# Kernel tuning notes

Hardware: AMD Instinct MI355X
Metric: run time of the kernel (lower is better)

Reference implementation:

```python
import jax, jax.numpy as jnp
import numpy as np

WIN = 8          # window side
N = WIN * WIN    # tokens per window = 64
C = 180          # channels
H = 6            # heads
D = C // H       # head dim = 30


def _relative_index():
    coords = jnp.stack(jnp.meshgrid(jnp.arange(WIN), jnp.arange(WIN), indexing='ij'))
    coords = coords.reshape(2, -1)                       # (2, N)
    rel = coords[:, :, None] - coords[:, None, :]        # (2, N, N)
    idx = (rel[0] + WIN - 1) * (2 * WIN - 1) + (rel[1] + WIN - 1)
    return idx.reshape(-1)                               # (N*N,) int


def setup_inputs() -> dict:
    key = jax.random.key(0)
    ks = jax.random.split(key, 6)
    B, WNum = 4096, 1024
    windows = jax.random.normal(ks[0], (B, N, C), dtype=jnp.float32)
    mask = jax.random.normal(ks[1], (WNum, N, N), dtype=jnp.float32)
    w_qkv = jax.random.normal(ks[2], (C, 3 * C), dtype=jnp.float32) * 0.02
    bias_table = jax.random.normal(ks[3], ((2 * WIN - 1) ** 2, H), dtype=jnp.float32) * 0.02
    w_proj = jax.random.normal(ks[4], (C, C), dtype=jnp.float32) * 0.02
    b_proj = jnp.zeros((C,), dtype=jnp.float32)
    return {"windows": windows, "mask": mask, "w_qkv": w_qkv,
            "bias_table": bias_table, "w_proj": w_proj, "b_proj": b_proj}


def reference(windows, mask, w_qkv, bias_table, w_proj, b_proj):
    B, n, c = windows.shape
    WNum = mask.shape[0]
    rel_idx = _relative_index()

    # qkv projection: (B, N, 3C) -> (3, B, H, N, D)
    qkv = (windows @ w_qkv).reshape(B, n, 3, H, D).transpose(2, 0, 3, 1, 4)
    q, k, v = qkv[0], qkv[1], qkv[2]

    scale = 1.0 / jnp.sqrt(jnp.float32(D))
    scores = jnp.einsum('bhnd,bhmd->bhnm', q, k) * scale     # (B, H, N, N)

    # relative position bias gather: (N*N, H) -> (H, N, N)
    rel_bias = bias_table[rel_idx].reshape(n, n, H).transpose(2, 0, 1)
    scores = scores + rel_bias[None]

    # per-window mask add
    scores = scores.reshape(B // WNum, WNum, H, n, n) + mask[None, :, None, :, :]
    scores = scores.reshape(B, H, n, n)

    attn = jax.nn.softmax(scores, axis=-1)
    out = jnp.einsum('bhnm,bhmd->bhnd', attn, v)             # (B, H, N, D)
    z = out.transpose(0, 2, 1, 3).reshape(B, n, c)
    return z @ w_proj + b_proj
```

## Files before the change

### kernel.cpp

```cpp
#include <hip/hip_runtime.h>


typedef __bf16 bf16;
typedef bf16 bf16x8 __attribute__((ext_vector_type(8)));
typedef float f32x4 __attribute__((ext_vector_type(4)));

#define MFMA(a, b, c) __builtin_amdgcn_mfma_f32_16x16x32_bf16(a, b, c, 0, 0, 0)

__global__ void prep_w(const float* __restrict__ wqkv,
                       const float* __restrict__ wproj,
                       const float* __restrict__ btab,
                       bf16* __restrict__ wqkvT,
                       bf16* __restrict__ wprojT,
                       float* __restrict__ relb)
{
    const int idx = blockIdx.x * 256 + threadIdx.x;
    if (idx < 110592) {
        const int oc = idx / 192, kk = idx - oc * 192;
        const int h = oc / 96, r = oc - h * 96;
        const int sec = r >> 5, d = r & 31;
        wqkvT[idx] = (bf16)((kk < 180 && d < 30) ? wqkv[kk * 540 + sec * 180 + h * 30 + d] : 0.f);
    } else if (idx < 147456) {
        const int r = idx - 110592;
        const int n = r / 192, k = r - n * 192;
        wprojT[r] = (bf16)((n < 180 && k < 180) ? wproj[k * 180 + n] : 0.f);
    } else if (idx < 172032) {
        const int r = idx - 147456;
        const int h = r >> 12;
        const int ij = r & 4095;
        const int i = ij >> 6, j = ij & 63;
        const int rel = ((i >> 3) - (j >> 3) + 7) * 15 + ((i & 7) - (j & 7) + 7);
        relb[r] = btab[rel * 6 + h];
    }
}

__global__ __launch_bounds__(384, 4)
void swin_mfma(const float* __restrict__ xg_all,
               const float* __restrict__ mask_all,
               const float* __restrict__ bproj,
               const bf16* __restrict__ wqkvT,
               const bf16* __restrict__ wprojT,
               const float* __restrict__ relb,
               float* __restrict__ outg)
{
    __shared__ __align__(16) short xb[64 * 200];

    const int b    = blockIdx.x;
    const int tid  = threadIdx.x;
    const int w    = tid >> 6;
    const int lane = tid & 63;
    const int l15  = lane & 15;
    const int g    = lane >> 4;

    const float* xg    = xg_all + (size_t)b * 11520;
    const float* maskw = mask_all + (size_t)(b & 1023) * 4096;

    {
        float4 xv[7];
        #pragma unroll
        for (int u = 0; u < 7; u++)
            xv[u] = *reinterpret_cast<const float4*>(xg + 4 * (tid + 384 * u));
        float4 xt;
        if (tid < 192) xt = *reinterpret_cast<const float4*>(xg + 4 * (2688 + tid));
        for (int e = tid; e < 640; e += 384) {
            const int i = e / 10;
            ((unsigned*)(xb + i * 200 + 180))[e - i * 10] = 0u;
        }
        #pragma unroll
        for (int u = 0; u < 7; u++) {
            const int e = tid + 384 * u;
            const int i = e / 45;
            const int c = 4 * e - i * 180;
            const unsigned p0 = (unsigned)__builtin_bit_cast(unsigned short, (bf16)xv[u].x)
                              | ((unsigned)__builtin_bit_cast(unsigned short, (bf16)xv[u].y) << 16);
            const unsigned p1 = (unsigned)__builtin_bit_cast(unsigned short, (bf16)xv[u].z)
                              | ((unsigned)__builtin_bit_cast(unsigned short, (bf16)xv[u].w) << 16);
            *reinterpret_cast<unsigned*>(xb + i * 200 + c)     = p0;
            *reinterpret_cast<unsigned*>(xb + i * 200 + c + 2) = p1;
        }
        if (tid < 192) {
            const int e = 2688 + tid;
            const int i = e / 45;
            const int c = 4 * e - i * 180;
            const unsigned p0 = (unsigned)__builtin_bit_cast(unsigned short, (bf16)xt.x)
                              | ((unsigned)__builtin_bit_cast(unsigned short, (bf16)xt.y) << 16);
            const unsigned p1 = (unsigned)__builtin_bit_cast(unsigned short, (bf16)xt.z)
                              | ((unsigned)__builtin_bit_cast(unsigned short, (bf16)xt.w) << 16);
            *reinterpret_cast<unsigned*>(xb + i * 200 + c)     = p0;
            *reinterpret_cast<unsigned*>(xb + i * 200 + c + 2) = p1;
        }
    }
    __syncthreads();

    const bf16* wqh = wqkvT + (size_t)(w * 96) * 192;
    const int rowoff = l15 * 192 + 8 * g;

    bf16x8 qf[4], kf[4];
    {
        f32x4 aqk[4][4];
        #pragma unroll
        for (int ct = 0; ct < 4; ct++)
            #pragma unroll
            for (int tt = 0; tt < 4; tt++) aqk[ct][tt] = (f32x4)0.f;
        #pragma unroll
        for (int ks = 0; ks < 6; ks++) {
            bf16x8 xf[4];
            #pragma unroll
            for (int tt = 0; tt < 4; tt++)
                xf[tt] = *reinterpret_cast<const bf16x8*>(xb + (16 * tt + l15) * 200 + 32 * ks + 8 * g);
            __builtin_amdgcn_s_setprio(1);
            #pragma unroll
            for (int ct = 0; ct < 4; ct++) {
                const bf16x8 wf = *reinterpret_cast<const bf16x8*>(wqh + ct * 3072 + rowoff + 32 * ks);
                #pragma unroll
                for (int tt = 0; tt < 4; tt++)
                    aqk[ct][tt] = MFMA(wf, xf[tt], aqk[ct][tt]);
            }
            __builtin_amdgcn_s_setprio(0);
        }
        #pragma unroll
        for (int tt = 0; tt < 4; tt++)
            #pragma unroll
            for (int s = 0; s < 8; s++) {
                qf[tt][s] = (bf16)(aqk[s >> 2][tt][s & 3] * 0.18257418583505537f);
                kf[tt][s] = (bf16)(aqk[2 + (s >> 2)][tt][s & 3]);
            }
    }
    __builtin_amdgcn_sched_barrier(0);

    bf16x8 pf[4][2];
    {
        const float* relh = relb + w * 4096;
        f32x4 bc[4];
        {
            const float* rbb = relh + l15 * 64 + 4 * g;
            const float* mkb = maskw + l15 * 64 + 4 * g;
            #pragma unroll
            for (int jt = 0; jt < 4; jt++) {
                const float4 rb = *reinterpret_cast<const float4*>(rbb + 16 * jt);
                const float4 mk = *reinterpret_cast<const float4*>(mkb + 16 * jt);
                bc[jt][0] = rb.x + mk.x; bc[jt][1] = rb.y + mk.y;
                bc[jt][2] = rb.z + mk.z; bc[jt][3] = rb.w + mk.w;
            }
        }
        #pragma unroll
        for (int it = 0; it < 4; it++) {
            f32x4 stj[4];
            __builtin_amdgcn_s_setprio(1);
            #pragma unroll
            for (int jt = 0; jt < 4; jt++) stj[jt] = MFMA(kf[jt], qf[it], bc[jt]);
            __builtin_amdgcn_s_setprio(0);

            f32x4 bn[4];
            if (it < 3) {
                const int i1 = 16 * (it + 1) + l15;
                const float* rbb = relh + i1 * 64 + 4 * g;
                const float* mkb = maskw + i1 * 64 + 4 * g;
                #pragma unroll
                for (int jt = 0; jt < 4; jt++) {
                    const float4 rb = *reinterpret_cast<const float4*>(rbb + 16 * jt);
                    const float4 mk = *reinterpret_cast<const float4*>(mkb + 16 * jt);
                    bn[jt][0] = rb.x + mk.x; bn[jt][1] = rb.y + mk.y;
                    bn[jt][2] = rb.z + mk.z; bn[jt][3] = rb.w + mk.w;
                }
            }

            float sum = 0.f;
            #pragma unroll
            for (int jt = 0; jt < 4; jt++) {
                const float e0 = __expf(stj[jt][0]);
                const float e1 = __expf(stj[jt][1]);
                const float e2 = __expf(stj[jt][2]);
                const float e3 = __expf(stj[jt][3]);
                stj[jt][0] = e0; stj[jt][1] = e1; stj[jt][2] = e2; stj[jt][3] = e3;
                sum += (e0 + e1) + (e2 + e3);
            }
            sum += __shfl_xor(sum, 16);
            sum += __shfl_xor(sum, 32);
            const float inv = 1.0f / sum;
            #pragma unroll
            for (int k2 = 0; k2 < 2; k2++)
                #pragma unroll
                for (int s = 0; s < 8; s++)
                    pf[it][k2][s] = (bf16)(stj[2 * k2 + (s >> 2)][s & 3] * inv);

            if (it < 3) {
                #pragma unroll
                for (int jt = 0; jt < 4; jt++) bc[jt] = bn[jt];
            }
        }
    }
    __builtin_amdgcn_sched_barrier(0);

    bf16x8 vf[2][2];
    {
        f32x4 av[4][2];
        #pragma unroll
        for (int tt = 0; tt < 4; tt++) { av[tt][0] = (f32x4)0.f; av[tt][1] = (f32x4)0.f; }
        #pragma unroll
        for (int ks = 0; ks < 6; ks++) {
            bf16x8 xf[4];
            #pragma unroll
            for (int tt = 0; tt < 4; tt++)
                xf[tt] = *reinterpret_cast<const bf16x8*>(xb + (16 * tt + l15) * 200 + 32 * ks + 8 * g);
            __builtin_amdgcn_s_setprio(1);
            #pragma unroll
            for (int cv = 0; cv < 2; cv++) {
                const bf16x8 wf = *reinterpret_cast<const bf16x8*>(wqh + (4 + cv) * 3072 + rowoff + 32 * ks);
                #pragma unroll
                for (int tt = 0; tt < 4; tt++)
                    av[tt][cv] = MFMA(xf[tt], wf, av[tt][cv]);
            }
            __builtin_amdgcn_s_setprio(0);
        }
        #pragma unroll
        for (int cv = 0; cv < 2; cv++)
            #pragma unroll
            for (int k2 = 0; k2 < 2; k2++)
                #pragma unroll
                for (int s = 0; s < 8; s++)
                    vf[cv][k2][s] = (bf16)(av[2 * k2 + (s >> 2)][cv][s & 3]);
    }
    __builtin_amdgcn_sched_barrier(0);

    f32x4 zacc[4][2];
    #pragma unroll
    for (int it = 0; it < 4; it++) { zacc[it][0] = (f32x4)0.f; zacc[it][1] = (f32x4)0.f; }
    __builtin_amdgcn_s_setprio(1);
    #pragma unroll
    for (int k2 = 0; k2 < 2; k2++)
        #pragma unroll
        for (int cv = 0; cv < 2; cv++)
            #pragma unroll
            for (int it = 0; it < 4; it++)
                zacc[it][cv] = MFMA(pf[it][k2], vf[cv][k2], zacc[it][cv]);
    __builtin_amdgcn_s_setprio(0);

    __syncthreads();
    #pragma unroll
    for (int cv = 0; cv < 2; cv++) {
        const int d = 16 * cv + l15;
        if (d < 30) {
            #pragma unroll
            for (int it = 0; it < 4; it++)
                #pragma unroll
                for (int r = 0; r < 4; r++)
                    xb[(16 * it + 4 * g + r) * 200 + w * 30 + d] =
                        __builtin_bit_cast(short, (bf16)zacc[it][cv][r]);
        }
    }
    __syncthreads();

    f32x4 pa[4][2];
    #pragma unroll
    for (int mt = 0; mt < 4; mt++) { pa[mt][0] = (f32x4)0.f; pa[mt][1] = (f32x4)0.f; }
    #pragma unroll
    for (int ks = 0; ks < 6; ks++) {
        bf16x8 zf[4];
        #pragma unroll
        for (int mt = 0; mt < 4; mt++)
            zf[mt] = *reinterpret_cast<const bf16x8*>(xb + (16 * mt + l15) * 200 + 32 * ks + 8 * g);
        __builtin_amdgcn_s_setprio(1);
        #pragma unroll
        for (int q2 = 0; q2 < 2; q2++) {
            const bf16x8 wf = *reinterpret_cast<const bf16x8*>(
                wprojT + ((2 * w + q2) * 16 + l15) * 192 + 32 * ks + 8 * g);
            #pragma unroll
            for (int mt = 0; mt < 4; mt++)
                pa[mt][q2] = MFMA(zf[mt], wf, pa[mt][q2]);
        }
        __builtin_amdgcn_s_setprio(0);
    }
    #pragma unroll
    for (int q2 = 0; q2 < 2; q2++) {
        const int n = (2 * w + q2) * 16 + l15;
        if (n < 180) {
            const float bn = bproj[n];
            float* const ob = outg + (size_t)b * 11520 + n;
            #pragma unroll
            for (int mt = 0; mt < 4; mt++)
                #pragma unroll
                for (int r = 0; r < 4; r++)
                    ob[(16 * mt + 4 * g + r) * 180] = pa[mt][q2][r] + bn;
        }
    }
}

extern "C" void kernel_launch(void* const* d_in, const int* in_sizes, int n_in,
                              void* d_out, int out_size, void* d_ws, size_t ws_size,
                              hipStream_t stream) {
    const float* windows = (const float*)d_in[0];
    const float* mask    = (const float*)d_in[1];
    const float* wqkv    = (const float*)d_in[2];
    const float* btab    = (const float*)d_in[3];
    const float* wproj   = (const float*)d_in[4];
    const float* bproj   = (const float*)d_in[5];

    bf16*  wqkvT  = (bf16*)d_ws;
    bf16*  wprojT = (bf16*)((char*)d_ws + 221184);
    float* relb   = (float*)((char*)d_ws + 294912);

    hipLaunchKernelGGL(prep_w, dim3(672), dim3(256), 0, stream,
                       wqkv, wproj, btab, wqkvT, wprojT, relb);
    hipLaunchKernelGGL(swin_mfma, dim3(4096), dim3(384), 0, stream,
                       windows, mask, bproj, wqkvT, wprojT, relb, (float*)d_out);
}
```

Before: 285.9 us.

## Process four same-mask windows per block with double-buffered LDS prefetch

```diff
diff --git a/kernel.cpp b/kernel.cpp
--- a/kernel.cpp
+++ b/kernel.cpp
@@ -34,6 +34,11 @@
     }
 }
 
+__device__ __forceinline__ unsigned pack2(float a, float b) {
+    return (unsigned)__builtin_bit_cast(unsigned short, (bf16)a)
+         | ((unsigned)__builtin_bit_cast(unsigned short, (bf16)b) << 16);
+}
+
 __global__ __launch_bounds__(384, 4)
 void swin_mfma(const float* __restrict__ xg_all,
                const float* __restrict__ mask_all,
@@ -43,7 +48,7 @@
                const float* __restrict__ relb,
                float* __restrict__ outg)
 {
-    __shared__ __align__(16) short xb[64 * 200];
+    __shared__ __align__(16) short xb2[2][64 * 200];
 
     const int b    = blockIdx.x;
     const int tid  = threadIdx.x;
@@ -52,237 +57,267 @@
     const int l15  = lane & 15;
     const int g    = lane >> 4;
 
-    const float* xg    = xg_all + (size_t)b * 11520;
-    const float* maskw = mask_all + (size_t)(b & 1023) * 4096;
-
+    const float* maskw = mask_all + (size_t)b * 4096;
+    const bf16*  wqh   = wqkvT + (size_t)(w * 96) * 192;
+    const int rowoff   = l15 * 192 + 8 * g;
+    const float* relh  = relb + w * 4096;
+
+    for (int e = tid; e < 1280; e += 384) {
+        const int bi = (e >= 640) ? 1 : 0;
+        const int e2 = e - bi * 640;
+        const int i = e2 / 10;
+        ((unsigned*)(&xb2[bi][0] + i * 200 + 180))[e2 - i * 10] = 0u;
+    }
     {
+        const float* xg = xg_all + (size_t)b * 11520;
         float4 xv[7];
         #pragma unroll
         for (int u = 0; u < 7; u++)
             xv[u] = *reinterpret_cast<const float4*>(xg + 4 * (tid + 384 * u));
         float4 xt;
         if (tid < 192) xt = *reinterpret_cast<const float4*>(xg + 4 * (2688 + tid));
-        for (int e = tid; e < 640; e += 384) {
-            const int i = e / 10;
-            ((unsigned*)(xb + i * 200 + 180))[e - i * 10] = 0u;
-        }
         #pragma unroll
         for (int u = 0; u < 7; u++) {
             const int e = tid + 384 * u;
             const int i = e / 45;
             const int c = 4 * e - i * 180;
-            const unsigned p0 = (unsigned)__builtin_bit_cast(unsigned short, (bf16)xv[u].x)
-                              | ((unsigned)__builtin_bit_cast(unsigned short, (bf16)xv[u].y) << 16);
-            const unsigned p1 = (unsigned)__builtin_bit_cast(unsigned short, (bf16)xv[u].z)
-                              | ((unsigned)__builtin_bit_cast(unsigned short, (bf16)xv[u].w) << 16);
-            *reinterpret_cast<unsigned*>(xb + i * 200 + c)     = p0;
-            *reinterpret_cast<unsigned*>(xb + i * 200 + c + 2) = p1;
+            *reinterpret_cast<unsigned*>(&xb2[0][0] + i * 200 + c)     = pack2(xv[u].x, xv[u].y);
+            *reinterpret_cast<unsigned*>(&xb2[0][0] + i * 200 + c + 2) = pack2(xv[u].z, xv[u].w);
         }
         if (tid < 192) {
             const int e = 2688 + tid;
             const int i = e / 45;
             const int c = 4 * e - i * 180;
-            const unsigned p0 = (unsigned)__builtin_bit_cast(unsigned short, (bf16)xt.x)
-                              | ((unsigned)__builtin_bit_cast(unsigned short, (bf16)xt.y) << 16);
-            const unsigned p1 = (unsigned)__builtin_bit_cast(unsigned short, (bf16)xt.z)
-                              | ((unsigned)__builtin_bit_cast(unsigned short, (bf16)xt.w) << 16);
-            *reinterpret_cast<unsigned*>(xb + i * 200 + c)     = p0;
-            *reinterpret_cast<unsigned*>(xb + i * 200 + c + 2) = p1;
+            *reinterpret_cast<unsigned*>(&xb2[0][0] + i * 200 + c)     = pack2(xt.x, xt.y);
+            *reinterpret_cast<unsigned*>(&xb2[0][0] + i * 200 + c + 2) = pack2(xt.z, xt.w);
         }
     }
     __syncthreads();
 
-    const bf16* wqh = wqkvT + (size_t)(w * 96) * 192;
-    const int rowoff = l15 * 192 + 8 * g;
-
-    bf16x8 qf[4], kf[4];
-    {
-        f32x4 aqk[4][4];
-        #pragma unroll
-        for (int ct = 0; ct < 4; ct++)
-            #pragma unroll
-            for (int tt = 0; tt < 4; tt++) aqk[ct][tt] = (f32x4)0.f;
-        #pragma unroll
-        for (int ks = 0; ks < 6; ks++) {
-            bf16x8 xf[4];
+    int cur = 0;
+    #pragma unroll 1
+    for (int wi = 0; wi < 4; ++wi) {
+        short* const xb = &xb2[cur][0];
+        const int bw = b + 1024 * wi;
+
+        bf16x8 qf[4], kf[4];
+        {
+            f32x4 aqk[4][4];
+            #pragma unroll
+            for (int ct = 0; ct < 4; ct++)
+                #pragma unroll
+                for (int tt = 0; tt < 4; tt++) aqk[ct][tt] = (f32x4)0.f;
+            #pragma unroll
+            for (int ks = 0; ks < 6; ks++) {
+                bf16x8 xf[4];
+                #pragma unroll
+                for (int tt = 0; tt < 4; tt++)
+                    xf[tt] = *reinterpret_cast<const bf16x8*>(xb + (16 * tt + l15) * 200 + 32 * ks + 8 * g);
+                __builtin_amdgcn_s_setprio(1);
+                #pragma unroll
+                for (int ct = 0; ct < 4; ct++) {
+                    const bf16x8 wf = *reinterpret_cast<const bf16x8*>(wqh + ct * 3072 + rowoff + 32 * ks);
+                    #pragma unroll
+                    for (int tt = 0; tt < 4; tt++)
+                        aqk[ct][tt] = MFMA(wf, xf[tt], aqk[ct][tt]);
+                }
+                __builtin_amdgcn_s_setprio(0);
+            }
             #pragma unroll
             for (int tt = 0; tt < 4; tt++)
-                xf[tt] = *reinterpret_cast<const bf16x8*>(xb + (16 * tt + l15) * 200 + 32 * ks + 8 * g);
-            __builtin_amdgcn_s_setprio(1);
-            #pragma unroll
-            for (int ct = 0; ct < 4; ct++) {
-                const bf16x8 wf = *reinterpret_cast<const bf16x8*>(wqh + ct * 3072 + rowoff + 32 * ks);
-                #pragma unroll
-                for (int tt = 0; tt < 4; tt++)
-                    aqk[ct][tt] = MFMA(wf, xf[tt], aqk[ct][tt]);
-            }
-            __builtin_amdgcn_s_setprio(0);
-        }
-        #pragma unroll
-        for (int tt = 0; tt < 4; tt++)
-            #pragma unroll
-            for (int s = 0; s < 8; s++) {
-                qf[tt][s] = (bf16)(aqk[s >> 2][tt][s & 3] * 0.18257418583505537f);
-                kf[tt][s] = (bf16)(aqk[2 + (s >> 2)][tt][s & 3]);
-            }
-    }
-    __builtin_amdgcn_sched_barrier(0);
-
-    bf16x8 pf[4][2];
-    {
-        const float* relh = relb + w * 4096;
-        f32x4 bc[4];
+                #pragma unroll
+                for (int s = 0; s < 8; s++) {
+                    qf[tt][s] = (bf16)(aqk[s >> 2][tt][s & 3] * 0.18257418583505537f);
+                    kf[tt][s] = (bf16)(aqk[2 + (s >> 2)][tt][s & 3]);
+                }
+        }
+        __builtin_amdgcn_sched_barrier(0);
+
+        bf16x8 pf[4][2];
         {
-            const float* rbb = relh + l15 * 64 + 4 * g;
-            const float* mkb = maskw + l15 * 64 + 4 * g;
-            #pragma unroll
-            for (int jt = 0; jt < 4; jt++) {
-                const float4 rb = *reinterpret_cast<const float4*>(rbb + 16 * jt);
-                const float4 mk = *reinterpret_cast<const float4*>(mkb + 16 * jt);
-                bc[jt][0] = rb.x + mk.x; bc[jt][1] = rb.y + mk.y;
-                bc[jt][2] = rb.z + mk.z; bc[jt][3] = rb.w + mk.w;
-            }
-        }
-        #pragma unroll
-        for (int it = 0; it < 4; it++) {
-            f32x4 stj[4];
-            __builtin_amdgcn_s_setprio(1);
-            #pragma unroll
-            for (int jt = 0; jt < 4; jt++) stj[jt] = MFMA(kf[jt], qf[it], bc[jt]);
-            __builtin_amdgcn_s_setprio(0);
-
-            f32x4 bn[4];
-            if (it < 3) {
-                const int i1 = 16 * (it + 1) + l15;
-                const float* rbb = relh + i1 * 64 + 4 * g;
-                const float* mkb = maskw + i1 * 64 + 4 * g;
+            f32x4 bc[4];
+            {
+                const float* rbb = relh + l15 * 64 + 4 * g;
+                const float* mkb = maskw + l15 * 64 + 4 * g;
                 #pragma unroll
                 for (int jt = 0; jt < 4; jt++) {
                     const float4 rb = *reinterpret_cast<const float4*>(rbb + 16 * jt);
                     const float4 mk = *reinterpret_cast<const float4*>(mkb + 16 * jt);
-                    bn[jt][0] = rb.x + mk.x; bn[jt][1] = rb.y + mk.y;
-                    bn[jt][2] = rb.z + mk.z; bn[jt][3] = rb.w + mk.w;
-                }
-            }
-
-            float sum = 0.f;
-            #pragma unroll
-            for (int jt = 0; jt < 4; jt++) {
-                const float e0 = __expf(stj[jt][0]);
-                const float e1 = __expf(stj[jt][1]);
-                const float e2 = __expf(stj[jt][2]);
-                const float e3 = __expf(stj[jt][3]);
-                stj[jt][0] = e0; stj[jt][1] = e1; stj[jt][2] = e2; stj[jt][3] = e3;
-                sum += (e0 + e1) + (e2 + e3);
-            }
-            sum += __shfl_xor(sum, 16);
-            sum += __shfl_xor(sum, 32);
-            const float inv = 1.0f / sum;
-            #pragma unroll
-            for (int k2 = 0; k2 < 2; k2++)
-                #pragma unroll
-                for (int s = 0; s < 8; s++)
-                    pf[it][k2][s] = (bf16)(stj[2 * k2 + (s >> 2)][s & 3] * inv);
-
-            if (it < 3) {
-                #pragma unroll
-                for (int jt = 0; jt < 4; jt++) bc[jt] = bn[jt];
-            }
-        }
-    }
-    __builtin_amdgcn_sched_barrier(0);
-
-    bf16x8 vf[2][2];
-    {
-        f32x4 av[4][2];
-        #pragma unroll
-        for (int tt = 0; tt < 4; tt++) { av[tt][0] = (f32x4)0.f; av[tt][1] = (f32x4)0.f; }
+                    bc[jt][0] = rb.x + mk.x; bc[jt][1] = rb.y + mk.y;
+                    bc[jt][2] = rb.z + mk.z; bc[jt][3] = rb.w + mk.w;
+                }
+            }
+            #pragma unroll
+            for (int it = 0; it < 4; it++) {
+                f32x4 stj[4];
+                __builtin_amdgcn_s_setprio(1);
+                #pragma unroll
+                for (int jt = 0; jt < 4; jt++) stj[jt] = MFMA(kf[jt], qf[it], bc[jt]);
+                __builtin_amdgcn_s_setprio(0);
+
+                f32x4 bn[4];
+                if (it < 3) {
+                    const int i1 = 16 * (it + 1) + l15;
+                    const float* rbb = relh + i1 * 64 + 4 * g;
+                    const float* mkb = maskw + i1 * 64 + 4 * g;
+                    #pragma unroll
+                    for (int jt = 0; jt < 4; jt++) {
+                        const float4 rb = *reinterpret_cast<const float4*>(rbb + 16 * jt);
+                        const float4 mk = *reinterpret_cast<const float4*>(mkb + 16 * jt);
+                        bn[jt][0] = rb.x + mk.x; bn[jt][1] = rb.y + mk.y;
+                        bn[jt][2] = rb.z + mk.z; bn[jt][3] = rb.w + mk.w;
+                    }
+                }
+
+                float sum = 0.f;
+                #pragma unroll
+                for (int jt = 0; jt < 4; jt++) {
+                    const float e0 = __expf(stj[jt][0]);
+                    const float e1 = __expf(stj[jt][1]);
+                    const float e2 = __expf(stj[jt][2]);
+                    const float e3 = __expf(stj[jt][3]);
+                    stj[jt][0] = e0; stj[jt][1] = e1; stj[jt][2] = e2; stj[jt][3] = e3;
+                    sum += (e0 + e1) + (e2 + e3);
+                }
+                sum += __shfl_xor(sum, 16);
+                sum += __shfl_xor(sum, 32);
+                const float inv = 1.0f / sum;
+                #pragma unroll
+                for (int k2 = 0; k2 < 2; k2++)
+                    #pragma unroll
+                    for (int s = 0; s < 8; s++)
+                        pf[it][k2][s] = (bf16)(stj[2 * k2 + (s >> 2)][s & 3] * inv);
+
+                if (it < 3) {
+                    #pragma unroll
+                    for (int jt = 0; jt < 4; jt++) bc[jt] = bn[jt];
+                }
+            }
+        }
+        __builtin_amdgcn_sched_barrier(0);
+
+        bf16x8 vf[2][2];
+        {
+            f32x4 av[4][2];
+            #pragma unroll
+            for (int tt = 0; tt < 4; tt++) { av[tt][0] = (f32x4)0.f; av[tt][1] = (f32x4)0.f; }
+            #pragma unroll
+            for (int ks = 0; ks < 6; ks++) {
+                bf16x8 xf[4];
+                #pragma unroll
+                for (int tt = 0; tt < 4; tt++)
+                    xf[tt] = *reinterpret_cast<const bf16x8*>(xb + (16 * tt + l15) * 200 + 32 * ks + 8 * g);
+                __builtin_amdgcn_s_setprio(1);
+                #pragma unroll
+                for (int cv = 0; cv < 2; cv++) {
+                    const bf16x8 wf = *reinterpret_cast<const bf16x8*>(wqh + (4 + cv) * 3072 + rowoff + 32 * ks);
+                    #pragma unroll
+                    for (int tt = 0; tt < 4; tt++)
+                        av[tt][cv] = MFMA(xf[tt], wf, av[tt][cv]);
+                }
+                __builtin_amdgcn_s_setprio(0);
+            }
+            #pragma unroll
+            for (int cv = 0; cv < 2; cv++)
+                #pragma unroll
+                for (int k2 = 0; k2 < 2; k2++)
+                    #pragma unroll
+                    for (int s = 0; s < 8; s++)
+                        vf[cv][k2][s] = (bf16)(av[2 * k2 + (s >> 2)][cv][s & 3]);
+        }
+        __builtin_amdgcn_sched_barrier(0);
+
+        f32x4 zacc[4][2];
+        #pragma unroll
+        for (int it = 0; it < 4; it++) { zacc[it][0] = (f32x4)0.f; zacc[it][1] = (f32x4)0.f; }
+        __builtin_amdgcn_s_setprio(1);
+        #pragma unroll
+        for (int k2 = 0; k2 < 2; k2++)
+            #pragma unroll
+            for (int cv = 0; cv < 2; cv++)
+                #pragma unroll
+                for (int it = 0; it < 4; it++)
+                    zacc[it][cv] = MFMA(pf[it][k2], vf[cv][k2], zacc[it][cv]);
+        __builtin_amdgcn_s_setprio(0);
+
+        __syncthreads();
+        #pragma unroll
+        for (int cv = 0; cv < 2; cv++) {
+            const int d = 16 * cv + l15;
+            if (d < 30) {
+                #pragma unroll
+                for (int it = 0; it < 4; it++)
+                    #pragma unroll
+                    for (int r = 0; r < 4; r++)
+                        xb[(16 * it + 4 * g + r) * 200 + w * 30 + d] =
+                            __builtin_bit_cast(short, (bf16)zacc[it][cv][r]);
+            }
+        }
+        __syncthreads();
+
+        float4 nxv[7], nxt;
+        if (wi < 3) {
+            const float* xgn = xg_all + (size_t)(bw + 1024) * 11520;
+            #pragma unroll
+            for (int u = 0; u < 7; u++)
+                nxv[u] = *reinterpret_cast<const float4*>(xgn + 4 * (tid + 384 * u));
+            if (tid < 192) nxt = *reinterpret_cast<const float4*>(xgn + 4 * (2688 + tid));
+        }
+
+        f32x4 pa[4][2];
+        #pragma unroll
+        for (int mt = 0; mt < 4; mt++) { pa[mt][0] = (f32x4)0.f; pa[mt][1] = (f32x4)0.f; }
         #pragma unroll
         for (int ks = 0; ks < 6; ks++) {
-            bf16x8 xf[4];
-            #pragma unroll
-            for (int tt = 0; tt < 4; tt++)
-                xf[tt] = *reinterpret_cast<const bf16x8*>(xb + (16 * tt + l15) * 200 + 32 * ks + 8 * g);
+            bf16x8 zf[4];
+            #pragma unroll
+            for (int mt = 0; mt < 4; mt++)
+                zf[mt] = *reinterpret_cast<const bf16x8*>(xb + (16 * mt + l15) * 200 + 32 * ks + 8 * g);
             __builtin_amdgcn_s_setprio(1);
             #pragma unroll
-            for (int cv = 0; cv < 2; cv++) {
-                const bf16x8 wf = *reinterpret_cast<const bf16x8*>(wqh + (4 + cv) * 3072 + rowoff + 32 * ks);
-                #pragma unroll
-                for (int tt = 0; tt < 4; tt++)
-                    av[tt][cv] = MFMA(xf[tt], wf, av[tt][cv]);
+            for (int q2 = 0; q2 < 2; q2++) {
+                const bf16x8 wf = *reinterpret_cast<const bf16x8*>(
+                    wprojT + ((2 * w + q2) * 16 + l15) * 192 + 32 * ks + 8 * g);
+                #pragma unroll
+                for (int mt = 0; mt < 4; mt++)
+                    pa[mt][q2] = MFMA(zf[mt], wf, pa[mt][q2]);
             }
             __builtin_amdgcn_s_setprio(0);
         }
         #pragma unroll
-        for (int cv = 0; cv < 2; cv++)
-            #pragma unroll
-            for (int k2 = 0; k2 < 2; k2++)
-                #pragma unroll
-                for (int s = 0; s < 8; s++)
-                    vf[cv][k2][s] = (bf16)(av[2 * k2 + (s >> 2)][cv][s & 3]);
-    }
-    __builtin_amdgcn_sched_barrier(0);
-
-    f32x4 zacc[4][2];
-    #pragma unroll
-    for (int it = 0; it < 4; it++) { zacc[it][0] = (f32x4)0.f; zacc[it][1] = (f32x4)0.f; }
-    __builtin_amdgcn_s_setprio(1);
-    #pragma unroll
-    for (int k2 = 0; k2 < 2; k2++)
-        #pragma unroll
-        for (int cv = 0; cv < 2; cv++)
-            #pragma unroll
-            for (int it = 0; it < 4; it++)
-                zacc[it][cv] = MFMA(pf[it][k2], vf[cv][k2], zacc[it][cv]);
-    __builtin_amdgcn_s_setprio(0);
-
-    __syncthreads();
-    #pragma unroll
-    for (int cv = 0; cv < 2; cv++) {
-        const int d = 16 * cv + l15;
-        if (d < 30) {
-            #pragma unroll
-            for (int it = 0; it < 4; it++)
-                #pragma unroll
-                for (int r = 0; r < 4; r++)
-                    xb[(16 * it + 4 * g + r) * 200 + w * 30 + d] =
-                        __builtin_bit_cast(short, (bf16)zacc[it][cv][r]);
-        }
-    }
-    __syncthreads();
-
-    f32x4 pa[4][2];
-    #pragma unroll
-    for (int mt = 0; mt < 4; mt++) { pa[mt][0] = (f32x4)0.f; pa[mt][1] = (f32x4)0.f; }
-    #pragma unroll
-    for (int ks = 0; ks < 6; ks++) {
-        bf16x8 zf[4];
-        #pragma unroll
-        for (int mt = 0; mt < 4; mt++)
-            zf[mt] = *reinterpret_cast<const bf16x8*>(xb + (16 * mt + l15) * 200 + 32 * ks + 8 * g);
-        __builtin_amdgcn_s_setprio(1);
-        #pragma unroll
         for (int q2 = 0; q2 < 2; q2++) {
-            const bf16x8 wf = *reinterpret_cast<const bf16x8*>(
-                wprojT + ((2 * w + q2) * 16 + l15) * 192 + 32 * ks + 8 * g);
-            #pragma unroll
-            for (int mt = 0; mt < 4; mt++)
-                pa[mt][q2] = MFMA(zf[mt], wf, pa[mt][q2]);
-        }
-        __builtin_amdgcn_s_setprio(0);
-    }
-    #pragma unroll
-    for (int q2 = 0; q2 < 2; q2++) {
-        const int n = (2 * w + q2) * 16 + l15;
-        if (n < 180) {
-            const float bn = bproj[n];
-            float* const ob = outg + (size_t)b * 11520 + n;
-            #pragma unroll
-            for (int mt = 0; mt < 4; mt++)
-                #pragma unroll
-                for (int r = 0; r < 4; r++)
-                    ob[(16 * mt + 4 * g + r) * 180] = pa[mt][q2][r] + bn;
-        }
+            const int n = (2 * w + q2) * 16 + l15;
+            if (n < 180) {
+                const float bn = bproj[n];
+                float* const ob = outg + (size_t)bw * 11520 + n;
+                #pragma unroll
+                for (int mt = 0; mt < 4; mt++)
+                    #pragma unroll
+                    for (int r = 0; r < 4; r++)
+                        ob[(16 * mt + 4 * g + r) * 180] = pa[mt][q2][r] + bn;
+            }
+        }
+
+        if (wi < 3) {
+            short* const nb = &xb2[cur ^ 1][0];
+            #pragma unroll
+            for (int u = 0; u < 7; u++) {
+                const int e = tid + 384 * u;
+                const int i = e / 45;
+                const int c = 4 * e - i * 180;
+                *reinterpret_cast<unsigned*>(nb + i * 200 + c)     = pack2(nxv[u].x, nxv[u].y);
+                *reinterpret_cast<unsigned*>(nb + i * 200 + c + 2) = pack2(nxv[u].z, nxv[u].w);
+            }
+            if (tid < 192) {
+                const int e = 2688 + tid;
+                const int i = e / 45;
+                const int c = 4 * e - i * 180;
+                *reinterpret_cast<unsigned*>(nb + i * 200 + c)     = pack2(nxt.x, nxt.y);
+                *reinterpret_cast<unsigned*>(nb + i * 200 + c + 2) = pack2(nxt.z, nxt.w);
+            }
+        }
+        __syncthreads();
+        cur ^= 1;
     }
 }
 
@@ -302,6 +337,6 @@
 
     hipLaunchKernelGGL(prep_w, dim3(672), dim3(256), 0, stream,
                        wqkv, wproj, btab, wqkvT, wprojT, relb);
-    hipLaunchKernelGGL(swin_mfma, dim3(4096), dim3(384), 0, stream,
+    hipLaunchKernelGGL(swin_mfma, dim3(1024), dim3(384), 0, stream,
                        windows, mask, bproj, wqkvT, wprojT, relb, (float*)d_out);
 }
```

Measured after the change: 645.6 us. 126% more time.

## Add 3-wave kernel processing two heads per wave with global z scratch

Applied to the files above, without the earlier changes.

```diff
diff --git a/kernel.cpp b/kernel.cpp
--- a/kernel.cpp
+++ b/kernel.cpp
@@ -34,14 +34,264 @@
     }
 }
 
+__device__ __forceinline__ unsigned pack2(float a, float b) {
+    return (unsigned)__builtin_bit_cast(unsigned short, (bf16)a)
+         | ((unsigned)__builtin_bit_cast(unsigned short, (bf16)b) << 16);
+}
+
+__global__ __launch_bounds__(192, 4)
+void swin_mfma3(const float* __restrict__ xg_all,
+                const float* __restrict__ mask_all,
+                const float* __restrict__ bproj,
+                const bf16* __restrict__ wqkvT,
+                const bf16* __restrict__ wprojT,
+                const float* __restrict__ relb,
+                bf16* __restrict__ zws,
+                float* __restrict__ outg)
+{
+    __shared__ __align__(16) short xb[64 * 200];
+
+    const int b    = blockIdx.x;
+    const int tid  = threadIdx.x;
+    const int wq   = tid >> 6;
+    const int lane = tid & 63;
+    const int l15  = lane & 15;
+    const int g    = lane >> 4;
+
+    const float* xg    = xg_all + (size_t)b * 11520;
+    const float* maskw = mask_all + (size_t)(b & 1023) * 4096;
+    bf16* const  zw    = zws + (size_t)b * 12288;
+
+    {
+        float4 xv[15];
+        #pragma unroll
+        for (int u = 0; u < 15; u++)
+            xv[u] = *reinterpret_cast<const float4*>(xg + 4 * (tid + 192 * u));
+        for (int e = tid; e < 640; e += 192) {
+            const int i = e / 10;
+            ((unsigned*)(xb + i * 200 + 180))[e - i * 10] = 0u;
+        }
+        #pragma unroll
+        for (int u = 0; u < 15; u++) {
+            const int e = tid + 192 * u;
+            const int i = e / 45;
+            const int c = 4 * e - i * 180;
+            *reinterpret_cast<unsigned*>(xb + i * 200 + c)     = pack2(xv[u].x, xv[u].y);
+            *reinterpret_cast<unsigned*>(xb + i * 200 + c + 2) = pack2(xv[u].z, xv[u].w);
+        }
+    }
+    __syncthreads();
+
+    #pragma unroll 1
+    for (int hh = 0; hh < 2; ++hh) {
+        const int h = 2 * wq + hh;
+        const bf16* wqh = wqkvT + (size_t)(h * 96) * 192;
+        const float* relh = relb + h * 4096;
+        const int rowoff = l15 * 192 + 8 * g;
+
+        bf16x8 qf[4], kf[4];
+        {
+            f32x4 aqk[4][4];
+            #pragma unroll
+            for (int ct = 0; ct < 4; ct++)
+                #pragma unroll
+                for (int tt = 0; tt < 4; tt++) aqk[ct][tt] = (f32x4)0.f;
+            #pragma unroll
+            for (int ks = 0; ks < 6; ks++) {
+                bf16x8 xf[4];
+                #pragma unroll
+                for (int tt = 0; tt < 4; tt++)
+                    xf[tt] = *reinterpret_cast<const bf16x8*>(xb + (16 * tt + l15) * 200 + 32 * ks + 8 * g);
+                __builtin_amdgcn_s_setprio(1);
+                #pragma unroll
+                for (int ct = 0; ct < 4; ct++) {
+                    const bf16x8 wf = *reinterpret_cast<const bf16x8*>(wqh + ct * 3072 + rowoff + 32 * ks);
+                    #pragma unroll
+                    for (int tt = 0; tt < 4; tt++)
+                        aqk[ct][tt] = MFMA(wf, xf[tt], aqk[ct][tt]);
+                }
+                __builtin_amdgcn_s_setprio(0);
+            }
+            #pragma unroll
+            for (int tt = 0; tt < 4; tt++)
+                #pragma unroll
+                for (int s = 0; s < 8; s++) {
+                    qf[tt][s] = (bf16)(aqk[s >> 2][tt][s & 3] * 0.18257418583505537f);
+                    kf[tt][s] = (bf16)(aqk[2 + (s >> 2)][tt][s & 3]);
+                }
+        }
+        __builtin_amdgcn_sched_barrier(0);
+
+        bf16x8 pf[4][2];
+        {
+            f32x4 bc[4];
+            {
+                const float* rbb = relh + l15 * 64 + 4 * g;
+                const float* mkb = maskw + l15 * 64 + 4 * g;
+                #pragma unroll
+                for (int jt = 0; jt < 4; jt++) {
+                    const float4 rb = *reinterpret_cast<const float4*>(rbb + 16 * jt);
+                    const float4 mk = *reinterpret_cast<const float4*>(mkb + 16 * jt);
+                    bc[jt][0] = rb.x + mk.x; bc[jt][1] = rb.y + mk.y;
+                    bc[jt][2] = rb.z + mk.z; bc[jt][3] = rb.w + mk.w;
+                }
+            }
+            #pragma unroll
+            for (int it = 0; it < 4; it++) {
+                f32x4 stj[4];
+                __builtin_amdgcn_s_setprio(1);
+                #pragma unroll
+                for (int jt = 0; jt < 4; jt++) stj[jt] = MFMA(kf[jt], qf[it], bc[jt]);
+                __builtin_amdgcn_s_setprio(0);
+
+                f32x4 bn[4];
+                if (it < 3) {
+                    const int i1 = 16 * (it + 1) + l15;
+                    const float* rbb = relh + i1 * 64 + 4 * g;
+                    const float* mkb = maskw + i1 * 64 + 4 * g;
+                    #pragma unroll
+                    for (int jt = 0; jt < 4; jt++) {
+                        const float4 rb = *reinterpret_cast<const float4*>(rbb + 16 * jt);
+                        const float4 mk = *reinterpret_cast<const float4*>(mkb + 16 * jt);
+                        bn[jt][0] = rb.x + mk.x; bn[jt][1] = rb.y + mk.y;
+                        bn[jt][2] = rb.z + mk.z; bn[jt][3] = rb.w + mk.w;
+                    }
+                }
+
+                float sum = 0.f;
+                #pragma unroll
+                for (int jt = 0; jt < 4; jt++) {
+                    const float e0 = __expf(stj[jt][0]);
+                    const float e1 = __expf(stj[jt][1]);
+                    const float e2 = __expf(stj[jt][2]);
+                    const float e3 = __expf(stj[jt][3]);
+                    stj[jt][0] = e0; stj[jt][1] = e1; stj[jt][2] = e2; stj[jt][3] = e3;
+                    sum += (e0 + e1) + (e2 + e3);
+                }
+                sum += __shfl_xor(sum, 16);
+                sum += __shfl_xor(sum, 32);
+                const float inv = 1.0f / sum;
+                #pragma unroll
+                for (int k2 = 0; k2 < 2; k2++)
+                    #pragma unroll
+                    for (int s = 0; s < 8; s++)
+                        pf[it][k2][s] = (bf16)(stj[2 * k2 + (s >> 2)][s & 3] * inv);
+
+                if (it < 3) {
+                    #pragma unroll
+                    for (int jt = 0; jt < 4; jt++) bc[jt] = bn[jt];
+                }
+            }
+        }
+        __builtin_amdgcn_sched_barrier(0);
+
+        bf16x8 vf[2][2];
+        {
+            f32x4 av[4][2];
+            #pragma unroll
+            for (int tt = 0; tt < 4; tt++) { av[tt][0] = (f32x4)0.f; av[tt][1] = (f32x4)0.f; }
+            #pragma unroll
+            for (int ks = 0; ks < 6; ks++) {
+                bf16x8 xf[4];
+                #pragma unroll
+                for (int tt = 0; tt < 4; tt++)
+                    xf[tt] = *reinterpret_cast<const bf16x8*>(xb + (16 * tt + l15) * 200 + 32 * ks + 8 * g);
+                __builtin_amdgcn_s_setprio(1);
+                #pragma unroll
+                for (int cv = 0; cv < 2; cv++) {
+                    const bf16x8 wf = *reinterpret_cast<const bf16x8*>(wqh + (4 + cv) * 3072 + rowoff + 32 * ks);
+                    #pragma unroll
+                    for (int tt = 0; tt < 4; tt++)
+                        av[tt][cv] = MFMA(xf[tt], wf, av[tt][cv]);
+                }
+                __builtin_amdgcn_s_setprio(0);
+            }
+            #pragma unroll
+            for (int cv = 0; cv < 2; cv++)
+                #pragma unroll
+                for (int k2 = 0; k2 < 2; k2++)
+                    #pragma unroll
+                    for (int s = 0; s < 8; s++)
+                        vf[cv][k2][s] = (bf16)(av[2 * k2 + (s >> 2)][cv][s & 3]);
+        }
+        __builtin_amdgcn_sched_barrier(0);
+
+        f32x4 zacc[4][2];
+        #pragma unroll
+        for (int it = 0; it < 4; it++) { zacc[it][0] = (f32x4)0.f; zacc[it][1] = (f32x4)0.f; }
+        __builtin_amdgcn_s_setprio(1);
+        #pragma unroll
+        for (int k2 = 0; k2 < 2; k2++)
+            #pragma unroll
+            for (int cv = 0; cv < 2; cv++)
+                #pragma unroll
+                for (int it = 0; it < 4; it++)
+                    zacc[it][cv] = MFMA(pf[it][k2], vf[cv][k2], zacc[it][cv]);
+        __builtin_amdgcn_s_setprio(0);
+
+        #pragma unroll
+        for (int cv = 0; cv < 2; cv++) {
+            const int d = 16 * cv + l15;
+            if (d < 30) {
+                #pragma unroll
+                for (int it = 0; it < 4; it++)
+                    #pragma unroll
+                    for (int r = 0; r < 4; r++)
+                        zw[(16 * it + 4 * g + r) * 192 + h * 30 + d] = (bf16)zacc[it][cv][r];
+            }
+        }
+        __builtin_amdgcn_sched_barrier(0);
+    }
+    __syncthreads();
+
+    {
+        f32x4 pa[4][4];
+        #pragma unroll
+        for (int mt = 0; mt < 4; mt++)
+            #pragma unroll
+            for (int q3 = 0; q3 < 4; q3++) pa[mt][q3] = (f32x4)0.f;
+        #pragma unroll
+        for (int ks = 0; ks < 6; ks++) {
+            bf16x8 zf[4];
+            #pragma unroll
+            for (int mt = 0; mt < 4; mt++)
+                zf[mt] = *reinterpret_cast<const bf16x8*>(zw + (16 * mt + l15) * 192 + 32 * ks + 8 * g);
+            __builtin_amdgcn_s_setprio(1);
+            #pragma unroll
+            for (int q3 = 0; q3 < 4; q3++) {
+                const int nt = 4 * wq + q3;
+                const bf16x8 wf = *reinterpret_cast<const bf16x8*>(
+                    wprojT + (nt * 16 + l15) * 192 + 32 * ks + 8 * g);
+                #pragma unroll
+                for (int mt = 0; mt < 4; mt++)
+                    pa[mt][q3] = MFMA(zf[mt], wf, pa[mt][q3]);
+            }
+            __builtin_amdgcn_s_setprio(0);
+        }
+        #pragma unroll
+        for (int q3 = 0; q3 < 4; q3++) {
+            const int n = (4 * wq + q3) * 16 + l15;
+            if (n < 180) {
+                const float bn = bproj[n];
+                float* const ob = outg + (size_t)b * 11520 + n;
+                #pragma unroll
+                for (int mt = 0; mt < 4; mt++)
+                    #pragma unroll
+                    for (int r = 0; r < 4; r++)
+                        ob[(16 * mt + 4 * g + r) * 180] = pa[mt][q3][r] + bn;
+            }
+        }
+    }
+}
+
 __global__ __launch_bounds__(384, 4)
-void swin_mfma(const float* __restrict__ xg_all,
-               const float* __restrict__ mask_all,
-               const float* __restrict__ bproj,
-               const bf16* __restrict__ wqkvT,
-               const bf16* __restrict__ wprojT,
-               const float* __restrict__ relb,
-               float* __restrict__ outg)
+void swin_mfma6(const float* __restrict__ xg_all,
+                const float* __restrict__ mask_all,
+                const float* __restrict__ bproj,
+                const bf16* __restrict__ wqkvT,
+                const bf16* __restrict__ wprojT,
+                const float* __restrict__ relb,
+                float* __restrict__ outg)
 {
     __shared__ __align__(16) short xb[64 * 200];
 
@@ -71,23 +321,15 @@
             const int e = tid + 384 * u;
             const int i = e / 45;
             const int c = 4 * e - i * 180;
-            const unsigned p0 = (unsigned)__builtin_bit_cast(unsigned short, (bf16)xv[u].x)
-                              | ((unsigned)__builtin_bit_cast(unsigned short, (bf16)xv[u].y) << 16);
-            const unsigned p1 = (unsigned)__builtin_bit_cast(unsigned short, (bf16)xv[u].z)
-                              | ((unsigned)__builtin_bit_cast(unsigned short, (bf16)xv[u].w) << 16);
-            *reinterpret_cast<unsigned*>(xb + i * 200 + c)     = p0;
-            *reinterpret_cast<unsigned*>(xb + i * 200 + c + 2) = p1;
+            *reinterpret_cast<unsigned*>(xb + i * 200 + c)     = pack2(xv[u].x, xv[u].y);
+            *reinterpret_cast<unsigned*>(xb + i * 200 + c + 2) = pack2(xv[u].z, xv[u].w);
         }
         if (tid < 192) {
             const int e = 2688 + tid;
             const int i = e / 45;
             const int c = 4 * e - i * 180;
-            const unsigned p0 = (unsigned)__builtin_bit_cast(unsigned short, (bf16)xt.x)
-                              | ((unsigned)__builtin_bit_cast(unsigned short, (bf16)xt.y) << 16);
-            const unsigned p1 = (unsigned)__builtin_bit_cast(unsigned short, (bf16)xt.z)
-                              | ((unsigned)__builtin_bit_cast(unsigned short, (bf16)xt.w) << 16);
-            *reinterpret_cast<unsigned*>(xb + i * 200 + c)     = p0;
-            *reinterpret_cast<unsigned*>(xb + i * 200 + c + 2) = p1;
+            *reinterpret_cast<unsigned*>(xb + i * 200 + c)     = pack2(xt.x, xt.y);
+            *reinterpret_cast<unsigned*>(xb + i * 200 + c + 2) = pack2(xt.z, xt.w);
         }
     }
     __syncthreads();
@@ -299,9 +541,17 @@
     bf16*  wqkvT  = (bf16*)d_ws;
     bf16*  wprojT = (bf16*)((char*)d_ws + 221184);
     float* relb   = (float*)((char*)d_ws + 294912);
+    bf16*  zws    = (bf16*)((char*)d_ws + 393216);
+
+    const bool ws_ok = ws_size >= (size_t)393216 + (size_t)4096 * 12288 * 2;
 
     hipLaunchKernelGGL(prep_w, dim3(672), dim3(256), 0, stream,
                        wqkv, wproj, btab, wqkvT, wprojT, relb);
-    hipLaunchKernelGGL(swin_mfma, dim3(4096), dim3(384), 0, stream,
-                       windows, mask, bproj, wqkvT, wprojT, relb, (float*)d_out);
+    if (ws_ok) {
+        hipLaunchKernelGGL(swin_mfma3, dim3(4096), dim3(192), 0, stream,
+                           windows, mask, bproj, wqkvT, wprojT, relb, zws, (float*)d_out);
+    } else {
+        hipLaunchKernelGGL(swin_mfma6, dim3(4096), dim3(384), 0, stream,
+                           windows, mask, bproj, wqkvT, wprojT, relb, (float*)d_out);
+    }
 }
```

New measurement: 471.4 us. +64.9%, slower.

## Compute V before softmax and fuse PV MFMA per row tile

Applied to the files above, without the earlier changes.

```diff
diff --git a/kernel.cpp b/kernel.cpp
--- a/kernel.cpp
+++ b/kernel.cpp
@@ -34,6 +34,11 @@
     }
 }
 
+__device__ __forceinline__ unsigned pack2(float a, float b) {
+    return (unsigned)__builtin_bit_cast(unsigned short, (bf16)a)
+         | ((unsigned)__builtin_bit_cast(unsigned short, (bf16)b) << 16);
+}
+
 __global__ __launch_bounds__(384, 4)
 void swin_mfma(const float* __restrict__ xg_all,
                const float* __restrict__ mask_all,
@@ -71,23 +76,15 @@
             const int e = tid + 384 * u;
             const int i = e / 45;
             const int c = 4 * e - i * 180;
-            const unsigned p0 = (unsigned)__builtin_bit_cast(unsigned short, (bf16)xv[u].x)
-                              | ((unsigned)__builtin_bit_cast(unsigned short, (bf16)xv[u].y) << 16);
-            const unsigned p1 = (unsigned)__builtin_bit_cast(unsigned short, (bf16)xv[u].z)
-                              | ((unsigned)__builtin_bit_cast(unsigned short, (bf16)xv[u].w) << 16);
-            *reinterpret_cast<unsigned*>(xb + i * 200 + c)     = p0;
-            *reinterpret_cast<unsigned*>(xb + i * 200 + c + 2) = p1;
+            *reinterpret_cast<unsigned*>(xb + i * 200 + c)     = pack2(xv[u].x, xv[u].y);
+            *reinterpret_cast<unsigned*>(xb + i * 200 + c + 2) = pack2(xv[u].z, xv[u].w);
         }
         if (tid < 192) {
             const int e = 2688 + tid;
             const int i = e / 45;
             const int c = 4 * e - i * 180;
-            const unsigned p0 = (unsigned)__builtin_bit_cast(unsigned short, (bf16)xt.x)
-                              | ((unsigned)__builtin_bit_cast(unsigned short, (bf16)xt.y) << 16);
-            const unsigned p1 = (unsigned)__builtin_bit_cast(unsigned short, (bf16)xt.z)
-                              | ((unsigned)__builtin_bit_cast(unsigned short, (bf16)xt.w) << 16);
-            *reinterpret_cast<unsigned*>(xb + i * 200 + c)     = p0;
-            *reinterpret_cast<unsigned*>(xb + i * 200 + c + 2) = p1;
+            *reinterpret_cast<unsigned*>(xb + i * 200 + c)     = pack2(xt.x, xt.y);
+            *reinterpret_cast<unsigned*>(xb + i * 200 + c + 2) = pack2(xt.z, xt.w);
         }
     }
     __syncthreads();
@@ -128,113 +125,90 @@
     }
     __builtin_amdgcn_sched_barrier(0);
 
-    bf16x8 pf[4][2];
+    bf16x8 vf[2][2];
+    {
+        f32x4 av[4][2];
+        #pragma unroll
+        for (int tt = 0; tt < 4; tt++) { av[tt][0] = (f32x4)0.f; av[tt][1] = (f32x4)0.f; }
+        #pragma unroll
+        for (int ks = 0; ks < 6; ks++) {
+            bf16x8 xf[4];
+            #pragma unroll
+            for (int tt = 0; tt < 4; tt++)
+                xf[tt] = *reinterpret_cast<const bf16x8*>(xb + (16 * tt + l15) * 200 + 32 * ks + 8 * g);
+            __builtin_amdgcn_s_setprio(1);
+            #pragma unroll
+            for (int cv = 0; cv < 2; cv++) {
+                const bf16x8 wf = *reinterpret_cast<const bf16x8*>(wqh + (4 + cv) * 3072 + rowoff + 32 * ks);
+                #pragma unroll
+                for (int tt = 0; tt < 4; tt++)
+                    av[tt][cv] = MFMA(xf[tt], wf, av[tt][cv]);
+            }
+            __builtin_amdgcn_s_setprio(0);
+        }
+        #pragma unroll
+        for (int cv = 0; cv < 2; cv++)
+            #pragma unroll
+            for (int k2 = 0; k2 < 2; k2++)
+                #pragma unroll
+                for (int s = 0; s < 8; s++)
+                    vf[cv][k2][s] = (bf16)(av[2 * k2 + (s >> 2)][cv][s & 3]);
+    }
+    __builtin_amdgcn_sched_barrier(0);
+
+    f32x4 zacc[4][2];
+    #pragma unroll
+    for (int it = 0; it < 4; it++) { zacc[it][0] = (f32x4)0.f; zacc[it][1] = (f32x4)0.f; }
     {
         const float* relh = relb + w * 4096;
-        f32x4 bc[4];
-        {
-            const float* rbb = relh + l15 * 64 + 4 * g;
-            const float* mkb = maskw + l15 * 64 + 4 * g;
+        #pragma unroll
+        for (int it = 0; it < 4; it++) {
+            const int i = 16 * it + l15;
+            const float* rbb = relh + i * 64 + 4 * g;
+            const float* mkb = maskw + i * 64 + 4 * g;
+            float4 rb[4], mk[4];
             #pragma unroll
             for (int jt = 0; jt < 4; jt++) {
-                const float4 rb = *reinterpret_cast<const float4*>(rbb + 16 * jt);
-                const float4 mk = *reinterpret_cast<const float4*>(mkb + 16 * jt);
-                bc[jt][0] = rb.x + mk.x; bc[jt][1] = rb.y + mk.y;
-                bc[jt][2] = rb.z + mk.z; bc[jt][3] = rb.w + mk.w;
-            }
-        }
-        #pragma unroll
-        for (int it = 0; it < 4; it++) {
+                rb[jt] = *reinterpret_cast<const float4*>(rbb + 16 * jt);
+                mk[jt] = *reinterpret_cast<const float4*>(mkb + 16 * jt);
+            }
+
             f32x4 stj[4];
             __builtin_amdgcn_s_setprio(1);
             #pragma unroll
-            for (int jt = 0; jt < 4; jt++) stj[jt] = MFMA(kf[jt], qf[it], bc[jt]);
-            __builtin_amdgcn_s_setprio(0);
-
-            f32x4 bn[4];
-            if (it < 3) {
-                const int i1 = 16 * (it + 1) + l15;
-                const float* rbb = relh + i1 * 64 + 4 * g;
-                const float* mkb = maskw + i1 * 64 + 4 * g;
-                #pragma unroll
-                for (int jt = 0; jt < 4; jt++) {
-                    const float4 rb = *reinterpret_cast<const float4*>(rbb + 16 * jt);
-                    const float4 mk = *reinterpret_cast<const float4*>(mkb + 16 * jt);
-                    bn[jt][0] = rb.x + mk.x; bn[jt][1] = rb.y + mk.y;
-                    bn[jt][2] = rb.z + mk.z; bn[jt][3] = rb.w + mk.w;
-                }
-            }
+            for (int jt = 0; jt < 4; jt++) stj[jt] = MFMA(kf[jt], qf[it], (f32x4)0.f);
+            __builtin_amdgcn_s_setprio(0);
 
             float sum = 0.f;
             #pragma unroll
             for (int jt = 0; jt < 4; jt++) {
-                const float e0 = __expf(stj[jt][0]);
-                const float e1 = __expf(stj[jt][1]);
-                const float e2 = __expf(stj[jt][2]);
-                const float e3 = __expf(stj[jt][3]);
+                const float e0 = __expf(stj[jt][0] + rb[jt].x + mk[jt].x);
+                const float e1 = __expf(stj[jt][1] + rb[jt].y + mk[jt].y);
+                const float e2 = __expf(stj[jt][2] + rb[jt].z + mk[jt].z);
+                const float e3 = __expf(stj[jt][3] + rb[jt].w + mk[jt].w);
                 stj[jt][0] = e0; stj[jt][1] = e1; stj[jt][2] = e2; stj[jt][3] = e3;
                 sum += (e0 + e1) + (e2 + e3);
             }
             sum += __shfl_xor(sum, 16);
             sum += __shfl_xor(sum, 32);
             const float inv = 1.0f / sum;
+
+            bf16x8 pfc[2];
             #pragma unroll
             for (int k2 = 0; k2 < 2; k2++)
                 #pragma unroll
                 for (int s = 0; s < 8; s++)
-                    pf[it][k2][s] = (bf16)(stj[2 * k2 + (s >> 2)][s & 3] * inv);
-
-            if (it < 3) {
-                #pragma unroll
-                for (int jt = 0; jt < 4; jt++) bc[jt] = bn[jt];
-            }
-        }
-    }
-    __builtin_amdgcn_sched_barrier(0);
-
-    bf16x8 vf[2][2];
-    {
-        f32x4 av[4][2];
-        #pragma unroll
-        for (int tt = 0; tt < 4; tt++) { av[tt][0] = (f32x4)0.f; av[tt][1] = (f32x4)0.f; }
-        #pragma unroll
-        for (int ks = 0; ks < 6; ks++) {
-            bf16x8 xf[4];
-            #pragma unroll
-            for (int tt = 0; tt < 4; tt++)
-                xf[tt] = *reinterpret_cast<const bf16x8*>(xb + (16 * tt + l15) * 200 + 32 * ks + 8 * g);
-            __builtin_amdgcn_s_setprio(1);
-            #pragma unroll
-            for (int cv = 0; cv < 2; cv++) {
-                const bf16x8 wf = *reinterpret_cast<const bf16x8*>(wqh + (4 + cv) * 3072 + rowoff + 32 * ks);
-                #pragma unroll
-                for (int tt = 0; tt < 4; tt++)
-                    av[tt][cv] = MFMA(xf[tt], wf, av[tt][cv]);
-            }
-            __builtin_amdgcn_s_setprio(0);
-        }
-        #pragma unroll
-        for (int cv = 0; cv < 2; cv++)
+                    pfc[k2][s] = (bf16)(stj[2 * k2 + (s >> 2)][s & 3] * inv);
+
+            __builtin_amdgcn_s_setprio(1);
             #pragma unroll
             for (int k2 = 0; k2 < 2; k2++)
                 #pragma unroll
-                for (int s = 0; s < 8; s++)
-                    vf[cv][k2][s] = (bf16)(av[2 * k2 + (s >> 2)][cv][s & 3]);
-    }
-    __builtin_amdgcn_sched_barrier(0);
-
-    f32x4 zacc[4][2];
-    #pragma unroll
-    for (int it = 0; it < 4; it++) { zacc[it][0] = (f32x4)0.f; zacc[it][1] = (f32x4)0.f; }
-    __builtin_amdgcn_s_setprio(1);
-    #pragma unroll
-    for (int k2 = 0; k2 < 2; k2++)
-        #pragma unroll
-        for (int cv = 0; cv < 2; cv++)
-            #pragma unroll
-            for (int it = 0; it < 4; it++)
-                zacc[it][cv] = MFMA(pf[it][k2], vf[cv][k2], zacc[it][cv]);
-    __builtin_amdgcn_s_setprio(0);
+                for (int cv = 0; cv < 2; cv++)
+                    zacc[it][cv] = MFMA(pfc[k2], vf[cv][k2], zacc[it][cv]);
+            __builtin_amdgcn_s_setprio(0);
+        }
+    }
 
     __syncthreads();
     #pragma unroll
```

After: 282.3 us (median of 2 runs). No clear change (-1.3%).
